# Kernel optimization log

Measured on AMD Instinct MI355X. Metric: run time of the kernel, lower is better.

Reference implementation:

```python
import jax, jax.numpy as jnp
import numpy as np

B, D, H, DEPTH = 1024, 1024, 1024, 4


def setup_inputs() -> dict:
    key = jax.random.key(0)
    k_x, k_w, k_ws, k_bs = jax.random.split(key, 4)
    x = jax.random.normal(k_x, (B, D), dtype=jnp.float32)
    W_enc = jax.random.normal(k_w, (D, H), dtype=jnp.float32) * 0.02
    b_enc = jnp.zeros((H,), dtype=jnp.float32)
    # per-layer CrossNet weights, matching keras random_normal init (stddev=0.05)
    ws = jax.random.normal(k_ws, (DEPTH, H, 1), dtype=jnp.float32) * 0.05
    bs = jax.random.normal(k_bs, (DEPTH, H, 1), dtype=jnp.float32) * 0.05
    return {"x": x, "W_enc": W_enc, "b_enc": b_enc, "ws": ws, "bs": bs}


def reference(x, W_enc, b_enc, ws, bs):
    # encoder Dense
    h = jnp.matmul(x, W_enc) + b_enc  # (B, H)
    x0 = h
    x_l = h
    depth = ws.shape[0]
    for l in range(depth):
        # original: (x0[:, :, None] * x_l[:, None, :]) @ w + b, squeezed.
        # outer[b,i,j] @ w  == x0[b,i] * sum_j x_l[b,j] * w[j]
        s = jnp.matmul(x_l, ws[l])            # (B, 1)
        residual = x0 * s + bs[l][:, 0]       # (B, H)
        x_l = residual + x_l
    return x_l
```

## Files before the change

kernel.cpp:

```cpp
#include <hip/hip_runtime.h>


#define B_SZ 1024
#define D_SZ 1024
#define H_SZ 1024
#define DEPTH 4

typedef _Float16 half4_t __attribute__((ext_vector_type(4)));
typedef _Float16 half8_t __attribute__((ext_vector_type(8)));
typedef float floatx4_t __attribute__((ext_vector_type(4)));

typedef const __attribute__((address_space(1))) unsigned int* gas_ptr;
typedef __attribute__((address_space(3))) unsigned int* las_ptr;

__device__ __forceinline__ void async_copy16(const void* g, void* l) {
    __builtin_amdgcn_global_load_lds((gas_ptr)g, (las_ptr)l, 16, 0, 0);
}

__global__ __launch_bounds__(256) void prep_kernel(
        const float* __restrict__ x, const float* __restrict__ W,
        const float* __restrict__ ws, const float* __restrict__ bs,
        _Float16* __restrict__ xh, _Float16* __restrict__ Wt,
        float* __restrict__ cvec, float* __restrict__ beta4) {
    const int b = blockIdx.x;
    const int t = threadIdx.x;
    if (b < 256) {
        __shared__ float S[64][65];
        const int k0 = (b >> 4) << 6;
        const int n0 = (b & 15) << 6;
#pragma unroll
        for (int i = 0; i < 4; ++i) {
            int idx = (i << 8) + t;
            int r = idx >> 4;
            int c4 = idx & 15;
            float4 v = *(const float4*)(W + (size_t)(k0 + r) * H_SZ + n0 + (c4 << 2));
            S[r][(c4 << 2) + 0] = v.x;
            S[r][(c4 << 2) + 1] = v.y;
            S[r][(c4 << 2) + 2] = v.z;
            S[r][(c4 << 2) + 3] = v.w;
        }
        __syncthreads();
#pragma unroll
        for (int i = 0; i < 4; ++i) {
            int idx = (i << 8) + t;
            int n = idx >> 4;
            int c4 = idx & 15;
            int k = c4 << 2;
            half4_t o;
            o.x = (_Float16)S[k + 0][n];
            o.y = (_Float16)S[k + 1][n];
            o.z = (_Float16)S[k + 2][n];
            o.w = (_Float16)S[k + 3][n];
            *(half4_t*)(Wt + (size_t)(n0 + n) * D_SZ + k0 + k) = o;
        }
    } else if (b < 512) {
        const int base = (b - 256) * 4096;
#pragma unroll
        for (int i = 0; i < 4; ++i) {
            int off = base + (((i << 8) + t) << 2);
            float4 v = *(const float4*)(x + off);
            half4_t o;
            o.x = (_Float16)v.x; o.y = (_Float16)v.y;
            o.z = (_Float16)v.z; o.w = (_Float16)v.w;
            *(half4_t*)(xh + off) = o;
        }
    } else {
        __shared__ float redc[4][3];
        const int j = t << 2;
        float4 b0 = *(const float4*)(bs + 0 * H_SZ + j);
        float4 b1 = *(const float4*)(bs + 1 * H_SZ + j);
        float4 b2 = *(const float4*)(bs + 2 * H_SZ + j);
        float4 b3 = *(const float4*)(bs + 3 * H_SZ + j);
        float4 w1 = *(const float4*)(ws + 1 * H_SZ + j);
        float4 w2 = *(const float4*)(ws + 2 * H_SZ + j);
        float4 w3 = *(const float4*)(ws + 3 * H_SZ + j);
        float4 pre1 = b0;
        float4 pre2 = {pre1.x + b1.x, pre1.y + b1.y, pre1.z + b1.z, pre1.w + b1.w};
        float4 pre3 = {pre2.x + b2.x, pre2.y + b2.y, pre2.z + b2.z, pre2.w + b2.w};
        float4 bt   = {pre3.x + b3.x, pre3.y + b3.y, pre3.z + b3.z, pre3.w + b3.w};
        *(float4*)(beta4 + j) = bt;
        float pp[3];
        pp[0] = pre1.x * w1.x + pre1.y * w1.y + pre1.z * w1.z + pre1.w * w1.w;
        pp[1] = pre2.x * w2.x + pre2.y * w2.y + pre2.z * w2.z + pre2.w * w2.w;
        pp[2] = pre3.x * w3.x + pre3.y * w3.y + pre3.z * w3.z + pre3.w * w3.w;
#pragma unroll
        for (int off = 32; off > 0; off >>= 1) {
#pragma unroll
            for (int l = 0; l < 3; ++l) pp[l] += __shfl_down(pp[l], off, 64);
        }
        if ((t & 63) == 0) {
#pragma unroll
            for (int l = 0; l < 3; ++l) redc[t >> 6][l] = pp[l];
        }
        __syncthreads();
        if (t == 0) {
            cvec[0] = 0.0f;
#pragma unroll
            for (int l = 0; l < 3; ++l)
                cvec[l + 1] = redc[0][l] + redc[1][l] + redc[2][l] + redc[3][l];
        }
    }
}

__global__ __launch_bounds__(512, 2) void gemm_kernel(
        const _Float16* __restrict__ xh, const _Float16* __restrict__ Wt,
        const float* __restrict__ b_enc, float* __restrict__ h) {
    __shared__ _Float16 As[2][32 * 128];
    __shared__ _Float16 Bs[2][64 * 128];
    const int tid  = threadIdx.x;
    const int lane = tid & 63;
    const int w    = tid >> 6;
    const int m0 = blockIdx.y << 5;
    const int n0 = blockIdx.x << 6;
    const int wm = (w >> 2) << 4;
    const int wn = (w & 3) << 4;

    const int ar = tid >> 4;
    const int ac = ((tid & 15) ^ (ar & 15)) << 3;
    const int br0 = tid >> 4;
    const int bc0 = ((tid & 15) ^ (br0 & 15)) << 3;
    const int br1 = br0 + 32;
    const int bc1 = ((tid & 15) ^ (br1 & 15)) << 3;
    const _Float16* aSrc  = xh + (size_t)(m0 + ar) * D_SZ + ac;
    const _Float16* bSrc0 = Wt + (size_t)(n0 + br0) * D_SZ + bc0;
    const _Float16* bSrc1 = Wt + (size_t)(n0 + br1) * D_SZ + bc1;

    const int ra = wm + (lane & 15);
    const int rb = wn + (lane & 15);
    const int q  = lane >> 4;

    floatx4_t acc = {0.0f, 0.0f, 0.0f, 0.0f};

    async_copy16(aSrc, &As[0][tid << 3]);
    async_copy16(bSrc0, &Bs[0][tid << 3]);
    async_copy16(bSrc1, &Bs[0][(tid + 512) << 3]);

    for (int it = 0; it < 8; ++it) {
        __syncthreads();
        if (it + 1 < 8) {
            int k0 = (it + 1) << 7;
            int buf = (it + 1) & 1;
            async_copy16(aSrc + k0, &As[buf][tid << 3]);
            async_copy16(bSrc0 + k0, &Bs[buf][tid << 3]);
            async_copy16(bSrc1 + k0, &Bs[buf][(tid + 512) << 3]);
        }
        const _Float16* Ab = As[it & 1];
        const _Float16* Bb = Bs[it & 1];
#pragma unroll
        for (int kk = 0; kk < 4; ++kk) {
            int l = (kk << 2) + q;
            half8_t af = *(const half8_t*)(Ab + ra * 128 + ((l ^ (ra & 15)) << 3));
            half8_t bf = *(const half8_t*)(Bb + rb * 128 + ((l ^ (rb & 15)) << 3));
            acc = __builtin_amdgcn_mfma_f32_16x16x32_f16(af, bf, acc, 0, 0, 0);
        }
    }

    const int col  = n0 + wn + (lane & 15);
    const int row0 = m0 + wm + (q << 2);
    const float be = b_enc[col];
#pragma unroll
    for (int r = 0; r < 4; ++r)
        h[(size_t)(row0 + r) * H_SZ + col] = acc[r] + be;
}

__global__ __launch_bounds__(256) void crossnet_kernel(
        float* __restrict__ h, const float* __restrict__ ws,
        const float* __restrict__ cvec, const float* __restrict__ beta4) {
    const int row = blockIdx.x;
    const int t = threadIdx.x;
    const int j = t << 2;
    float* hr = h + (size_t)row * H_SZ;

    float4 hv = *(const float4*)(hr + j);
    float x0[4] = {hv.x, hv.y, hv.z, hv.w};

    float p[DEPTH];
#pragma unroll
    for (int l = 0; l < DEPTH; ++l) {
        float4 wv = *(const float4*)(ws + l * H_SZ + j);
        p[l] = x0[0] * wv.x + x0[1] * wv.y + x0[2] * wv.z + x0[3] * wv.w;
    }
#pragma unroll
    for (int off = 32; off > 0; off >>= 1) {
#pragma unroll
        for (int l = 0; l < DEPTH; ++l) p[l] += __shfl_down(p[l], off, 64);
    }
    __shared__ float red[4][DEPTH];
    if ((t & 63) == 0) {
#pragma unroll
        for (int l = 0; l < DEPTH; ++l) red[t >> 6][l] = p[l];
    }
    __syncthreads();

    float sig = 1.0f;
#pragma unroll
    for (int l = 0; l < DEPTH; ++l) {
        float d = red[0][l] + red[1][l] + red[2][l] + red[3][l];
        float s = sig * d + cvec[l];
        sig += s;
    }
    float4 b4 = *(const float4*)(beta4 + j);
    float4 o = {x0[0] * sig + b4.x, x0[1] * sig + b4.y,
                x0[2] * sig + b4.z, x0[3] * sig + b4.w};
    *(float4*)(hr + j) = o;
}

extern "C" void kernel_launch(void* const* d_in, const int* in_sizes, int n_in,
                              void* d_out, int out_size, void* d_ws, size_t ws_size,
                              hipStream_t stream) {
    const float* x     = (const float*)d_in[0];
    const float* W_enc = (const float*)d_in[1];
    const float* b_enc = (const float*)d_in[2];
    const float* ws    = (const float*)d_in[3];
    const float* bs    = (const float*)d_in[4];
    float* out = (float*)d_out;

    _Float16* xh = (_Float16*)d_ws;
    _Float16* Wt = xh + (size_t)B_SZ * D_SZ;
    float* aux   = (float*)((char*)d_ws + 4u * 1024u * 1024u);
    float* cvec  = aux;
    float* beta4 = aux + 4;

    prep_kernel<<<513, 256, 0, stream>>>(x, W_enc, ws, bs, xh, Wt, cvec, beta4);
    dim3 grid(H_SZ / 64, B_SZ / 32);
    gemm_kernel<<<grid, 512, 0, stream>>>(xh, Wt, b_enc, out);
    crossnet_kernel<<<B_SZ, 256, 0, stream>>>(out, ws, cvec, beta4);
}
```

Measured before the change: 79.95 us.

## Fuse crossnet into GEMM epilogue via precomputed W·ws projections

Precomputes g_l = W_enc·ws_l in the prep kernel, so each row's crossnet dot products become x·g_l plus constant terms from b_enc. Each GEMM block computes its own rows' sigma scalars and writes the final output directly. This removes the separate crossnet kernel and its full read and rewrite of h. The cost is redundant per-block row dot products across the 16 column blocks, and fp16 rounding of g, which changes numerical precision.

```diff
diff --git a/kernel.cpp b/kernel.cpp
--- a/kernel.cpp
+++ b/kernel.cpp
@@ -19,9 +19,11 @@
 
 __global__ __launch_bounds__(256) void prep_kernel(
         const float* __restrict__ x, const float* __restrict__ W,
-        const float* __restrict__ ws, const float* __restrict__ bs,
+        const float* __restrict__ b_enc, const float* __restrict__ ws,
+        const float* __restrict__ bs,
         _Float16* __restrict__ xh, _Float16* __restrict__ Wt,
-        float* __restrict__ cvec, float* __restrict__ beta4) {
+        float* __restrict__ cvec, float* __restrict__ evec,
+        float* __restrict__ beta4, _Float16* __restrict__ gh) {
     const int b = blockIdx.x;
     const int t = threadIdx.x;
     if (b < 256) {
@@ -64,33 +66,39 @@
             o.z = (_Float16)v.z; o.w = (_Float16)v.w;
             *(half4_t*)(xh + off) = o;
         }
-    } else {
-        __shared__ float redc[4][3];
+    } else if (b == 512) {
+        __shared__ float redc[4][7];
         const int j = t << 2;
         float4 b0 = *(const float4*)(bs + 0 * H_SZ + j);
         float4 b1 = *(const float4*)(bs + 1 * H_SZ + j);
         float4 b2 = *(const float4*)(bs + 2 * H_SZ + j);
         float4 b3 = *(const float4*)(bs + 3 * H_SZ + j);
+        float4 w0 = *(const float4*)(ws + 0 * H_SZ + j);
         float4 w1 = *(const float4*)(ws + 1 * H_SZ + j);
         float4 w2 = *(const float4*)(ws + 2 * H_SZ + j);
         float4 w3 = *(const float4*)(ws + 3 * H_SZ + j);
+        float4 be = *(const float4*)(b_enc + j);
         float4 pre1 = b0;
         float4 pre2 = {pre1.x + b1.x, pre1.y + b1.y, pre1.z + b1.z, pre1.w + b1.w};
         float4 pre3 = {pre2.x + b2.x, pre2.y + b2.y, pre2.z + b2.z, pre2.w + b2.w};
         float4 bt   = {pre3.x + b3.x, pre3.y + b3.y, pre3.z + b3.z, pre3.w + b3.w};
         *(float4*)(beta4 + j) = bt;
-        float pp[3];
+        float pp[7];
         pp[0] = pre1.x * w1.x + pre1.y * w1.y + pre1.z * w1.z + pre1.w * w1.w;
         pp[1] = pre2.x * w2.x + pre2.y * w2.y + pre2.z * w2.z + pre2.w * w2.w;
         pp[2] = pre3.x * w3.x + pre3.y * w3.y + pre3.z * w3.z + pre3.w * w3.w;
+        pp[3] = be.x * w0.x + be.y * w0.y + be.z * w0.z + be.w * w0.w;
+        pp[4] = be.x * w1.x + be.y * w1.y + be.z * w1.z + be.w * w1.w;
+        pp[5] = be.x * w2.x + be.y * w2.y + be.z * w2.z + be.w * w2.w;
+        pp[6] = be.x * w3.x + be.y * w3.y + be.z * w3.z + be.w * w3.w;
 #pragma unroll
         for (int off = 32; off > 0; off >>= 1) {
 #pragma unroll
-            for (int l = 0; l < 3; ++l) pp[l] += __shfl_down(pp[l], off, 64);
+            for (int l = 0; l < 7; ++l) pp[l] += __shfl_down(pp[l], off, 64);
         }
         if ((t & 63) == 0) {
 #pragma unroll
-            for (int l = 0; l < 3; ++l) redc[t >> 6][l] = pp[l];
+            for (int l = 0; l < 7; ++l) redc[t >> 6][l] = pp[l];
         }
         __syncthreads();
         if (t == 0) {
@@ -98,15 +106,41 @@
 #pragma unroll
             for (int l = 0; l < 3; ++l)
                 cvec[l + 1] = redc[0][l] + redc[1][l] + redc[2][l] + redc[3][l];
-        }
-    }
-}
-
-__global__ __launch_bounds__(512, 2) void gemm_kernel(
+#pragma unroll
+            for (int l = 0; l < 4; ++l)
+                evec[l] = redc[0][3 + l] + redc[1][3 + l] +
+                          redc[2][3 + l] + redc[3][3 + l];
+        }
+    } else {
+        const int gb  = b - 513;
+        const int k0  = gb << 4;
+        const int dot = t >> 2;
+        const int row = k0 + (dot >> 2);
+        const int layer = dot & 3;
+        const int sub = t & 3;
+        const float* wr = W + (size_t)row * H_SZ + (sub << 8);
+        const float* wl = ws + layer * H_SZ + (sub << 8);
+        float acc = 0.0f;
+#pragma unroll 8
+        for (int n = 0; n < 256; n += 4) {
+            float4 a = *(const float4*)(wr + n);
+            float4 c = *(const float4*)(wl + n);
+            acc += a.x * c.x + a.y * c.y + a.z * c.z + a.w * c.w;
+        }
+        acc += __shfl_xor(acc, 1, 64);
+        acc += __shfl_xor(acc, 2, 64);
+        if (sub == 0) gh[layer * D_SZ + row] = (_Float16)acc;
+    }
+}
+
+__global__ __launch_bounds__(512, 2) void gemm_cross_kernel(
         const _Float16* __restrict__ xh, const _Float16* __restrict__ Wt,
-        const float* __restrict__ b_enc, float* __restrict__ h) {
+        const float* __restrict__ b_enc, const _Float16* __restrict__ gh,
+        const float* __restrict__ cvec, const float* __restrict__ evec,
+        const float* __restrict__ beta4, float* __restrict__ h) {
     __shared__ _Float16 As[2][32 * 128];
     __shared__ _Float16 Bs[2][64 * 128];
+    __shared__ float sigS[32];
     const int tid  = threadIdx.x;
     const int lane = tid & 63;
     const int w    = tid >> 6;
@@ -155,54 +189,69 @@
         }
     }
 
+    {
+        const int lr0 = w << 2;
+        const int ks  = lane << 4;
+        float dsum[4][4];
+#pragma unroll
+        for (int rr = 0; rr < 4; ++rr) {
+            const _Float16* xr = xh + (size_t)(m0 + lr0 + rr) * D_SZ + ks;
+            half8_t xa = *(const half8_t*)(xr);
+            half8_t xb = *(const half8_t*)(xr + 8);
+            float xs[16];
+#pragma unroll
+            for (int i = 0; i < 8; ++i) {
+                xs[i]     = (float)xa[i];
+                xs[8 + i] = (float)xb[i];
+            }
+#pragma unroll
+            for (int l = 0; l < 4; ++l) {
+                const _Float16* gr = gh + l * D_SZ + ks;
+                half8_t ga = *(const half8_t*)(gr);
+                half8_t gb = *(const half8_t*)(gr + 8);
+                float s = 0.0f;
+#pragma unroll
+                for (int i = 0; i < 8; ++i)
+                    s += xs[i] * (float)ga[i] + xs[8 + i] * (float)gb[i];
+                dsum[rr][l] = s;
+            }
+        }
+#pragma unroll
+        for (int off = 32; off > 0; off >>= 1)
+#pragma unroll
+            for (int rr = 0; rr < 4; ++rr)
+#pragma unroll
+                for (int l = 0; l < 4; ++l)
+                    dsum[rr][l] += __shfl_xor(dsum[rr][l], off, 64);
+        if (lane == 0) {
+            const float4 cv = *(const float4*)cvec;
+            const float4 ev = *(const float4*)evec;
+#pragma unroll
+            for (int rr = 0; rr < 4; ++rr) {
+                float dl[4] = {dsum[rr][0] + ev.x, dsum[rr][1] + ev.y,
+                               dsum[rr][2] + ev.z, dsum[rr][3] + ev.w};
+                const float cl[4] = {cv.x, cv.y, cv.z, cv.w};
+                float sig = 1.0f;
+#pragma unroll
+                for (int l = 0; l < 4; ++l) {
+                    float s = sig * dl[l] + cl[l];
+                    sig += s;
+                }
+                sigS[lr0 + rr] = sig;
+            }
+        }
+    }
+    __syncthreads();
+
     const int col  = n0 + wn + (lane & 15);
     const int row0 = m0 + wm + (q << 2);
-    const float be = b_enc[col];
-#pragma unroll
-    for (int r = 0; r < 4; ++r)
-        h[(size_t)(row0 + r) * H_SZ + col] = acc[r] + be;
-}
-
-__global__ __launch_bounds__(256) void crossnet_kernel(
-        float* __restrict__ h, const float* __restrict__ ws,
-        const float* __restrict__ cvec, const float* __restrict__ beta4) {
-    const int row = blockIdx.x;
-    const int t = threadIdx.x;
-    const int j = t << 2;
-    float* hr = h + (size_t)row * H_SZ;
-
-    float4 hv = *(const float4*)(hr + j);
-    float x0[4] = {hv.x, hv.y, hv.z, hv.w};
-
-    float p[DEPTH];
-#pragma unroll
-    for (int l = 0; l < DEPTH; ++l) {
-        float4 wv = *(const float4*)(ws + l * H_SZ + j);
-        p[l] = x0[0] * wv.x + x0[1] * wv.y + x0[2] * wv.z + x0[3] * wv.w;
-    }
-#pragma unroll
-    for (int off = 32; off > 0; off >>= 1) {
-#pragma unroll
-        for (int l = 0; l < DEPTH; ++l) p[l] += __shfl_down(p[l], off, 64);
-    }
-    __shared__ float red[4][DEPTH];
-    if ((t & 63) == 0) {
-#pragma unroll
-        for (int l = 0; l < DEPTH; ++l) red[t >> 6][l] = p[l];
-    }
-    __syncthreads();
-
-    float sig = 1.0f;
-#pragma unroll
-    for (int l = 0; l < DEPTH; ++l) {
-        float d = red[0][l] + red[1][l] + red[2][l] + red[3][l];
-        float s = sig * d + cvec[l];
-        sig += s;
-    }
-    float4 b4 = *(const float4*)(beta4 + j);
-    float4 o = {x0[0] * sig + b4.x, x0[1] * sig + b4.y,
-                x0[2] * sig + b4.z, x0[3] * sig + b4.w};
-    *(float4*)(hr + j) = o;
+    const float be  = b_enc[col];
+    const float bt4 = beta4[col];
+#pragma unroll
+    for (int r = 0; r < 4; ++r) {
+        float sig = sigS[wm + (q << 2) + r];
+        h[(size_t)(row0 + r) * H_SZ + col] = sig * (acc[r] + be) + bt4;
+    }
 }
 
 extern "C" void kernel_launch(void* const* d_in, const int* in_sizes, int n_in,
@@ -219,10 +268,13 @@
     _Float16* Wt = xh + (size_t)B_SZ * D_SZ;
     float* aux   = (float*)((char*)d_ws + 4u * 1024u * 1024u);
     float* cvec  = aux;
-    float* beta4 = aux + 4;
-
-    prep_kernel<<<513, 256, 0, stream>>>(x, W_enc, ws, bs, xh, Wt, cvec, beta4);
+    float* evec  = aux + 4;
+    float* beta4 = aux + 8;
+    _Float16* gh = (_Float16*)(aux + 8 + H_SZ);
+
+    prep_kernel<<<577, 256, 0, stream>>>(x, W_enc, b_enc, ws, bs,
+                                         xh, Wt, cvec, evec, beta4, gh);
     dim3 grid(H_SZ / 64, B_SZ / 32);
-    gemm_kernel<<<grid, 512, 0, stream>>>(xh, Wt, b_enc, out);
-    crossnet_kernel<<<B_SZ, 256, 0, stream>>>(out, ws, cvec, beta4);
-}
+    gemm_cross_kernel<<<grid, 512, 0, stream>>>(xh, Wt, b_enc, gh,
+                                                cvec, evec, beta4, out);
+}
```

New measurement: 102.8 us. 28.6% more time.
